# Optimization experiments

Hardware: AMD Instinct MI355X
Metric: run time of the kernel (lower is better)

The kernel has to match this reference:

```python
import jax, jax.numpy as jnp
import numpy as np

CODEBOOK_SIZE = 1024
CODEBOOK_DIM = 64
COMMITMENT_WEIGHT = 0.25
DECAY = 0.99
EPS = 1e-5


def setup_inputs() -> dict:
    key = jax.random.key(0)
    k1, k2, k3 = jax.random.split(key, 3)
    B, D, T = 32, CODEBOOK_DIM, 4096
    z = jax.random.normal(k1, (B, D, T), dtype=jnp.float32)
    embedding = jax.random.normal(k2, (CODEBOOK_SIZE, CODEBOOK_DIM), dtype=jnp.float32)
    cluster_size = jnp.zeros((CODEBOOK_SIZE,), dtype=jnp.float32)
    embed_avg = jax.random.normal(k3, (CODEBOOK_SIZE, CODEBOOK_DIM), dtype=jnp.float32)
    return {"z": z, "embedding": embedding, "cluster_size": cluster_size, "embed_avg": embed_avg}


def reference(z, embedding, cluster_size, embed_avg):
    # z: [B, D, T]; embedding/embed_avg: [K, D]; cluster_size: [K]
    B, D, T = z.shape
    K = embedding.shape[0]
    z_flat = jnp.transpose(z, (0, 2, 1)).reshape(-1, D)  # [N, D], N = B*T

    # squared-euclidean distances via expansion (matches torch cdist expansion)
    dist = (
        jnp.sum(z_flat * z_flat, axis=1, keepdims=True)
        + jnp.sum(embedding * embedding, axis=1)
        - 2.0 * (z_flat @ embedding.T)
    )  # [N, K]
    indices = jnp.argmin(dist, axis=1)  # [N] int

    # EMA updates (training path). one_hot.sum(0) -> segment count; one_hot.T @ z_flat -> segment sum
    counts = jax.ops.segment_sum(jnp.ones(z_flat.shape[0], dtype=z_flat.dtype), indices, num_segments=K)
    new_cluster_size = cluster_size * DECAY + (1.0 - DECAY) * counts
    embed_sum = jax.ops.segment_sum(z_flat, indices, num_segments=K)  # [K, D]
    new_embed_avg = embed_avg * DECAY + (1.0 - DECAY) * embed_sum
    n = jnp.sum(new_cluster_size)
    smoothed = (new_cluster_size + EPS) / (n + K * EPS) * n  # Laplace smoothing
    new_embedding = new_embed_avg / smoothed[:, None]  # [K, D]

    # quantize with the *updated* codebook (as in the torch in-place update)
    z_q_flat = new_embedding[indices]  # [N, D] gather
    loss = COMMITMENT_WEIGHT * jnp.mean((z_flat - jax.lax.stop_gradient(z_q_flat)) ** 2)
    # straight-through estimator
    z_q_flat = z_flat + jax.lax.stop_gradient(z_q_flat - z_flat)
    z_q = jnp.transpose(z_q_flat.reshape(B, T, D), (0, 2, 1))  # [B, D, T]
    return z_q, loss, indices.reshape(B, T)
```

## Files before the change

kernel.cpp:

```cpp
#include <hip/hip_runtime.h>

#define N_PTS 131072
#define TD 4096
#define DD 64
#define KK 1024
#define MARGIN_TH 2e-3f

typedef short bf16x8 __attribute__((ext_vector_type(8)));
typedef float f32x4  __attribute__((ext_vector_type(4)));

__device__ inline unsigned short f2bf(float f) {
    unsigned u = __float_as_uint(f);
    unsigned r = u + 0x7FFFu + ((u >> 16) & 1u);
    return (unsigned short)(r >> 16);
}
__device__ inline float bf2f(unsigned short h) {
    return __uint_as_float(((unsigned)h) << 16);
}

__global__ __launch_bounds__(256) void vq_prep(const float* __restrict__ z,
                                               unsigned short* __restrict__ zh,
                                               unsigned short* __restrict__ zl)
{
    __shared__ float tile[64][65];
    const int tid = threadIdx.x;
    const int b = blockIdx.x >> 6;
    const int t0 = (blockIdx.x & 63) * 64;

    const int d = tid >> 2, tq = tid & 3;
#pragma unroll
    for (int it = 0; it < 4; ++it) {
        const int tt = tq * 16 + it * 4;
        const float4 v = *(const float4*)(z + ((size_t)b * DD + d) * TD + t0 + tt);
        tile[d][tt] = v.x; tile[d][tt + 1] = v.y; tile[d][tt + 2] = v.z; tile[d][tt + 3] = v.w;
    }
    __syncthreads();

    const int p = tid >> 2, dg = tid & 3;
    bf16x8 h0, h1, l0, l1;
#pragma unroll
    for (int j = 0; j < 8; ++j) {
        const float v0 = -tile[dg * 16 + j][p];
        const unsigned short a = f2bf(v0);
        h0[j] = (short)a; l0[j] = (short)f2bf(v0 - bf2f(a));
        const float v1 = -tile[dg * 16 + 8 + j][p];
        const unsigned short c = f2bf(v1);
        h1[j] = (short)c; l1[j] = (short)f2bf(v1 - bf2f(c));
    }
    const size_t o = ((size_t)(b * TD + t0 + p)) * DD + dg * 16;
    *(bf16x8*)(zh + o) = h0;
    *(bf16x8*)(zh + o + 8) = h1;
    *(bf16x8*)(zl + o) = l0;
    *(bf16x8*)(zl + o + 8) = l1;
}

__global__ __launch_bounds__(256) void vq_eprep(const float* __restrict__ emb,
                                                unsigned short* __restrict__ efh,
                                                unsigned short* __restrict__ efl,
                                                float* __restrict__ halfnorm)
{
    const int k = blockIdx.x * 256 + threadIdx.x;
    if (k >= KK) return;
    const int t = k >> 4, col = k & 15;
    const float* e = emb + (size_t)k * DD;
    double s = 0.0;
#pragma unroll
    for (int d = 0; d < DD; ++d) {
        const float v = e[d];
        const double dv = (double)v;
        s = fma(dv, dv, s);
        const unsigned short h = f2bf(v);
        const int q = d >> 3, j = d & 7;
        const size_t pos = (size_t)t * 1024 + (q >> 2) * 512 + ((q & 3) * 16 + col) * 8 + j;
        efh[pos] = h;
        efl[pos] = f2bf(v - bf2f(h));
    }
    halfnorm[k] = (float)(0.5 * s);
}

__global__ __launch_bounds__(256, 6) void vq_screen_mfma(
    const unsigned short* __restrict__ zh, const unsigned short* __restrict__ zl,
    const unsigned short* __restrict__ efh, const unsigned short* __restrict__ efl,
    const float* __restrict__ hn,
    int* __restrict__ idx_ws, float* __restrict__ ind_out,
    int* __restrict__ nflag, int* __restrict__ flags)
{
    __shared__ __align__(16) unsigned short tiles[2][2048];

    const int tid  = threadIdx.x;
    const int lane = tid & 63;
    const int wv   = tid >> 6;
    const int quad = lane >> 4;
    const int col  = lane & 15;
    const int loff = lane * 8;
    const int pbase = blockIdx.x * 64 + wv * 16;

    const bf16x8* ph = (const bf16x8*)(zh + (size_t)(pbase + col) * DD + quad * 8);
    const bf16x8* pl = (const bf16x8*)(zl + (size_t)(pbase + col) * DD + quad * 8);
    const bf16x8 Ah0 = ph[0], Ah1 = ph[4];
    const bf16x8 Al0 = pl[0], Al1 = pl[4];

    const unsigned short* sg = (tid < 128) ? (efh + tid * 8) : (efl + (tid - 128) * 8);

    *(bf16x8*)(&tiles[0][tid * 8]) = *(const bf16x8*)(sg);
    float chn = hn[col];

    float best[4]  = {1e30f, 1e30f, 1e30f, 1e30f};
    float best2[4] = {1e30f, 1e30f, 1e30f, 1e30f};
    int   bidx[4]  = {0, 0, 0, 0};

    __syncthreads();

    for (int t = 0; t < KK / 16; ++t) {
        const int cur = t & 1;

        bf16x8 nr;
        float nhn = 0.f;
        if (t < 63) {
            nr = *(const bf16x8*)(sg + (size_t)(t + 1) * 1024);
            nhn = hn[(t + 1) * 16 + col];
        }

        const unsigned short* buf = &tiles[cur][0];
        const bf16x8 Bh0 = *(const bf16x8*)(buf + loff);
        const bf16x8 Bh1 = *(const bf16x8*)(buf + 512 + loff);
        const bf16x8 Bl0 = *(const bf16x8*)(buf + 1024 + loff);
        const bf16x8 Bl1 = *(const bf16x8*)(buf + 1536 + loff);

        if (t < 63) *(bf16x8*)(&tiles[cur ^ 1][tid * 8]) = nr;

        f32x4 p = {chn, chn, chn, chn};
        p = __builtin_amdgcn_mfma_f32_16x16x32_bf16(Ah0, Bh0, p, 0, 0, 0);
        p = __builtin_amdgcn_mfma_f32_16x16x32_bf16(Ah1, Bh1, p, 0, 0, 0);
        p = __builtin_amdgcn_mfma_f32_16x16x32_bf16(Al0, Bh0, p, 0, 0, 0);
        p = __builtin_amdgcn_mfma_f32_16x16x32_bf16(Al1, Bh1, p, 0, 0, 0);
        p = __builtin_amdgcn_mfma_f32_16x16x32_bf16(Ah0, Bl0, p, 0, 0, 0);
        p = __builtin_amdgcn_mfma_f32_16x16x32_bf16(Ah1, Bl1, p, 0, 0, 0);

        const int code = t * 16 + col;
#pragma unroll
        for (int r = 0; r < 4; ++r) {
            const float s = p[r];
            best2[r] = __builtin_amdgcn_fmed3f(best[r], best2[r], s);
            bidx[r] = (s < best[r]) ? code : bidx[r];
            best[r] = fminf(best[r], s);
        }

        __syncthreads();
        chn = nhn;
    }

#pragma unroll
    for (int off = 1; off < 16; off <<= 1) {
#pragma unroll
        for (int r = 0; r < 4; ++r) {
            const float ob  = __shfl_xor(best[r],  off, 64);
            const float ob2 = __shfl_xor(best2[r], off, 64);
            const int   oi  = __shfl_xor(bidx[r],  off, 64);
            const float nb2 = fminf(fminf(best2[r], ob2), fmaxf(best[r], ob));
            if (ob < best[r]) { best[r] = ob; bidx[r] = oi; }
            best2[r] = nb2;
        }
    }

    if (col == 0) {
#pragma unroll
        for (int r = 0; r < 4; ++r) {
            const int n0 = pbase + quad * 4 + r;
            idx_ws[n0] = bidx[r];
            ind_out[n0] = (float)bidx[r];
            if (best2[r] - best[r] < MARGIN_TH) {
                const int pos = atomicAdd(nflag, 1);
                flags[pos] = n0;
            }
        }
    }
}

__global__ __launch_bounds__(256) void vq_fallback(
    const float* __restrict__ z, const float* __restrict__ emb,
    int* __restrict__ idx_ws, float* __restrict__ ind_out,
    const int* __restrict__ nflag, const int* __restrict__ flags)
{
    __shared__ float zs[4][DD];
    const int total = *nflag;
    const int lane = threadIdx.x & 63;
    const int wid = threadIdx.x >> 6;
    const int gw = blockIdx.x * 4 + wid;

    for (int i = gw; i < total; i += gridDim.x * 4) {
        const int n = flags[i];
        const int b = n >> 12, t = n & 4095;
        zs[wid][lane] = z[((size_t)b * DD + lane) * TD + t];
        __builtin_amdgcn_s_waitcnt(0);
        double best = 1e300;
        int bi = KK;
        for (int kc = 0; kc < KK / 64; ++kc) {
            const int k = kc * 64 + lane;
            const float4* e = (const float4*)(emb + (size_t)k * DD);
            double dot = 0.0, nn = 0.0;
#pragma unroll
            for (int j = 0; j < 16; ++j) {
                float4 ev = e[j];
                double e0 = (double)ev.x, e1 = (double)ev.y, e2 = (double)ev.z, e3 = (double)ev.w;
                nn = fma(e0, e0, fma(e1, e1, fma(e2, e2, fma(e3, e3, nn))));
                dot = fma((double)zs[wid][4 * j + 0], e0,
                      fma((double)zs[wid][4 * j + 1], e1,
                      fma((double)zs[wid][4 * j + 2], e2,
                      fma((double)zs[wid][4 * j + 3], e3, dot))));
            }
            double s = 0.5 * nn - dot;
            if (s < best || (s == best && k < bi)) { best = s; bi = k; }
        }
        for (int off = 32; off > 0; off >>= 1) {
            double os = __shfl_down(best, off, 64);
            int oi = __shfl_down(bi, off, 64);
            if (os < best || (os == best && oi < bi)) { best = os; bi = oi; }
        }
        if (lane == 0) { idx_ws[n] = bi; ind_out[n] = (float)bi; }
    }
}

__global__ __launch_bounds__(256) void vq_hist(const int* __restrict__ idx_ws, int* __restrict__ hist)
{
    __shared__ int h[KK];
    for (int i = threadIdx.x; i < KK; i += 256) h[i] = 0;
    __syncthreads();
    const int base = blockIdx.x * 2048;
#pragma unroll
    for (int j = 0; j < 8; ++j)
        atomicAdd(&h[idx_ws[base + j * 256 + threadIdx.x]], 1);
    __syncthreads();
    for (int i = threadIdx.x; i < KK; i += 256)
        if (h[i]) atomicAdd(&hist[i], h[i]);
}

__global__ __launch_bounds__(1024) void vq_prefix_smo(
    const int* __restrict__ hist, const float* __restrict__ cs,
    int* __restrict__ cursor, float* __restrict__ rsmo)
{
    __shared__ int tmp[KK];
    __shared__ double dred[KK];
    const int k = threadIdx.x;
    const int c = hist[k];
    tmp[k] = c;
    const double ncs = 0.99 * (double)cs[k] + 0.01 * (double)c;
    dred[k] = ncs;
    __syncthreads();
    for (int off = 1; off < KK; off <<= 1) {
        int u = (k >= off) ? tmp[k - off] : 0;
        __syncthreads();
        tmp[k] += u;
        __syncthreads();
    }
    cursor[k] = tmp[k] - c;
    for (int s = 512; s > 0; s >>= 1) {
        if (k < s) dred[k] += dred[k + s];
        __syncthreads();
    }
    const double nsum = dred[0];
    const double smo = (ncs + 1e-5) / (nsum + (double)KK * 1e-5) * nsum;
    rsmo[k] = (float)(1.0 / smo);
}

__global__ __launch_bounds__(256) void vq_scatter(const int* __restrict__ idx_ws,
                                                  int* __restrict__ cursor, int* __restrict__ order)
{
    const int n = blockIdx.x * 256 + threadIdx.x;
    const int bi = idx_ws[n];
    const int pos = atomicAdd(&cursor[bi], 1);
    order[pos] = n;
}

__global__ __launch_bounds__(256) void vq_esum2(
    const unsigned short* __restrict__ zh, const unsigned short* __restrict__ zl,
    const int* __restrict__ idx_ws, const int* __restrict__ order,
    float* __restrict__ esum)
{
    const int tid = threadIdx.x;
    const int lane = tid & 63;
    const int w = tid >> 6;
    const int base = blockIdx.x * 256 + w * 64;

    const int pid_l = order[base + lane];
    const int code_l = idx_ws[pid_l];

    float v[64];
#pragma unroll
    for (int j = 0; j < 64; ++j) {
        const int pj = __shfl(pid_l, j, 64);
        const size_t o = (size_t)pj * DD + lane;
        v[j] = bf2f(zh[o]) + bf2f(zl[o]);
    }

    float racc = 0.f;
    int cur = __shfl(code_l, 0, 64);
#pragma unroll
    for (int j = 0; j < 64; ++j) {
        const int cj = __shfl(code_l, j, 64);
        if (cj != cur) {
            atomicAdd(&esum[(size_t)cur * DD + lane], -racc);
            racc = 0.f;
            cur = cj;
        }
        racc += v[j];
    }
    atomicAdd(&esum[(size_t)cur * DD + lane], -racc);
}

__global__ __launch_bounds__(256) void vq_newE(
    const float* __restrict__ avg, const float* __restrict__ esum,
    const float* __restrict__ rsmo, float* __restrict__ newE)
{
    const int j = blockIdx.x * 256 + threadIdx.x;
    newE[j] = (float)((0.99 * (double)avg[j] + 0.01 * (double)esum[j]) * (double)rsmo[j >> 6]);
}

__global__ __launch_bounds__(256) void vq_gather_loss(
    const float* __restrict__ z, const float* __restrict__ newE,
    const int* __restrict__ idx_ws, float* __restrict__ zq_out,
    double* __restrict__ loss_acc, int* __restrict__ done_cnt,
    float* __restrict__ loss_out)
{
    const int tid = threadIdx.x;
    const int n = blockIdx.x * 256 + tid;
    const int b = n >> 12;
    const int t = n & 4095;
    const float* zb = z + ((size_t)b * DD) * TD + t;
    float* ob = zq_out + ((size_t)b * DD) * TD + t;
    const int bi = idx_ws[n];
    const float* e = newE + (size_t)bi * DD;
    double acc = 0.0;
#pragma unroll
    for (int d = 0; d < DD; ++d) {
        float q = e[d];
        float zv = zb[(size_t)d * TD];
        ob[(size_t)d * TD] = q;
        float df = zv - q;
        acc = fma((double)df, (double)df, acc);
    }
    for (int off = 32; off > 0; off >>= 1) acc += __shfl_down(acc, off, 64);
    __shared__ double wsum[4];
    const int wid = tid >> 6, lane = tid & 63;
    if (lane == 0) wsum[wid] = acc;
    __syncthreads();
    if (tid == 0) {
        atomicAdd(loss_acc, wsum[0] + wsum[1] + wsum[2] + wsum[3]);
        __threadfence();
        const int prev = atomicAdd(done_cnt, 1);
        if (prev == gridDim.x - 1) {
            __threadfence();
            *loss_out = (float)(0.25 * (*loss_acc) / (double)(N_PTS * DD));
        }
    }
}

extern "C" void kernel_launch(void* const* d_in, const int* in_sizes, int n_in,
                              void* d_out, int out_size, void* d_ws, size_t ws_size,
                              hipStream_t stream) {
    const float* z    = (const float*)d_in[0];
    const float* emb  = (const float*)d_in[1];
    const float* cs   = (const float*)d_in[2];
    const float* avg  = (const float*)d_in[3];

    float* out      = (float*)d_out;
    float* zq_out   = out;
    float* loss_out = out + 8388608;
    float* ind_out  = out + 8388609;

    unsigned short* zh = (unsigned short*)d_out;
    unsigned short* zl = (unsigned short*)((char*)d_out + 16777216);

    char* ws = (char*)d_ws;
    int*            idx_ws   = (int*)ws;
    float*          newE     = (float*)(ws + 524288);
    float*          esum     = (float*)(ws + 786432);
    int*            hist     = (int*)(ws + 1048576);
    int*            nflag    = (int*)(ws + 1052672);
    int*            done_cnt = (int*)(ws + 1052676);
    double*         loss_acc = (double*)(ws + 1052680);
    float*          halfnorm = (float*)(ws + 1052688);
    int*            cursor   = (int*)(ws + 1056784);
    int*            flags    = (int*)(ws + 1060880);
    int*            order    = (int*)(ws + 1585168);
    unsigned short* efh      = (unsigned short*)(ws + 2109456);
    unsigned short* efl      = (unsigned short*)(ws + 2240528);
    float*          rsmo     = (float*)(ws + 2371600);

    hipMemsetAsync(ws + 786432, 0, 266256, stream);

    vq_prep<<<2048, 256, 0, stream>>>(z, zh, zl);
    vq_eprep<<<4, 256, 0, stream>>>(emb, efh, efl, halfnorm);
    vq_screen_mfma<<<N_PTS / 64, 256, 0, stream>>>(zh, zl, efh, efl, halfnorm,
                                                   idx_ws, ind_out, nflag, flags);
    vq_fallback<<<128, 256, 0, stream>>>(z, emb, idx_ws, ind_out, nflag, flags);
    vq_hist<<<64, 256, 0, stream>>>(idx_ws, hist);
    vq_prefix_smo<<<1, 1024, 0, stream>>>(hist, cs, cursor, rsmo);
    vq_scatter<<<N_PTS / 256, 256, 0, stream>>>(idx_ws, cursor, order);
    vq_esum2<<<N_PTS / 256, 256, 0, stream>>>(zh, zl, idx_ws, order, esum);
    vq_newE<<<256, 256, 0, stream>>>(avg, esum, rsmo, newE);
    vq_gather_loss<<<N_PTS / 256, 256, 0, stream>>>(z, newE, idx_ws, zq_out,
                                                    loss_acc, done_cnt, loss_out);
}
```

Baseline: 294.4 us.

## Use direct global-to-LDS loads with 4-deep staging and fuse codebook prep

The screening kernel now streams codebook tiles straight into LDS with global_load_lds across a 4-buffer ring. It keeps two tiles in flight and synchronises with vmcnt waits plus a single barrier per step, instead of a register round-trip and a trailing syncthreads. The half-norms are preloaded into shared memory once per block, and the codebook prep kernel is folded into vq_prep as extra blocks to save a launch. The cost is more LDS per block, which may limit occupancy, and the hand-written waitcnt ordering has to be correct.

```diff
diff --git a/kernel.cpp b/kernel.cpp
--- a/kernel.cpp
+++ b/kernel.cpp
@@ -18,12 +18,43 @@
     return __uint_as_float(((unsigned)h) << 16);
 }
 
+__device__ inline void gload_lds16(const unsigned short* g, unsigned short* l) {
+    __builtin_amdgcn_global_load_lds(
+        (const __attribute__((address_space(1))) unsigned int*)g,
+        (__attribute__((address_space(3))) unsigned int*)l, 16, 0, 0);
+}
+
 __global__ __launch_bounds__(256) void vq_prep(const float* __restrict__ z,
                                                unsigned short* __restrict__ zh,
-                                               unsigned short* __restrict__ zl)
+                                               unsigned short* __restrict__ zl,
+                                               const float* __restrict__ emb,
+                                               unsigned short* __restrict__ efh,
+                                               unsigned short* __restrict__ efl,
+                                               float* __restrict__ halfnorm)
 {
     __shared__ float tile[64][65];
     const int tid = threadIdx.x;
+
+    if (blockIdx.x >= 2048) {
+        const int k = (blockIdx.x - 2048) * 256 + tid;
+        const int t = k >> 4, col = k & 15;
+        const float* e = emb + (size_t)k * DD;
+        double s = 0.0;
+#pragma unroll
+        for (int d = 0; d < DD; ++d) {
+            const float v = e[d];
+            const double dv = (double)v;
+            s = fma(dv, dv, s);
+            const unsigned short h = f2bf(v);
+            const int q = d >> 3, j = d & 7;
+            const size_t pos = (size_t)t * 1024 + (q >> 2) * 512 + ((q & 3) * 16 + col) * 8 + j;
+            efh[pos] = h;
+            efl[pos] = f2bf(v - bf2f(h));
+        }
+        halfnorm[k] = (float)(0.5 * s);
+        return;
+    }
+
     const int b = blockIdx.x >> 6;
     const int t0 = (blockIdx.x & 63) * 64;
 
@@ -54,30 +85,6 @@
     *(bf16x8*)(zl + o + 8) = l1;
 }
 
-__global__ __launch_bounds__(256) void vq_eprep(const float* __restrict__ emb,
-                                                unsigned short* __restrict__ efh,
-                                                unsigned short* __restrict__ efl,
-                                                float* __restrict__ halfnorm)
-{
-    const int k = blockIdx.x * 256 + threadIdx.x;
-    if (k >= KK) return;
-    const int t = k >> 4, col = k & 15;
-    const float* e = emb + (size_t)k * DD;
-    double s = 0.0;
-#pragma unroll
-    for (int d = 0; d < DD; ++d) {
-        const float v = e[d];
-        const double dv = (double)v;
-        s = fma(dv, dv, s);
-        const unsigned short h = f2bf(v);
-        const int q = d >> 3, j = d & 7;
-        const size_t pos = (size_t)t * 1024 + (q >> 2) * 512 + ((q & 3) * 16 + col) * 8 + j;
-        efh[pos] = h;
-        efl[pos] = f2bf(v - bf2f(h));
-    }
-    halfnorm[k] = (float)(0.5 * s);
-}
-
 __global__ __launch_bounds__(256, 6) void vq_screen_mfma(
     const unsigned short* __restrict__ zh, const unsigned short* __restrict__ zl,
     const unsigned short* __restrict__ efh, const unsigned short* __restrict__ efl,
@@ -85,7 +92,8 @@
     int* __restrict__ idx_ws, float* __restrict__ ind_out,
     int* __restrict__ nflag, int* __restrict__ flags)
 {
-    __shared__ __align__(16) unsigned short tiles[2][2048];
+    __shared__ __align__(16) unsigned short tiles[4][2048];
+    __shared__ float hns[KK];
 
     const int tid  = threadIdx.x;
     const int lane = tid & 63;
@@ -100,55 +108,69 @@
     const bf16x8 Ah0 = ph[0], Ah1 = ph[4];
     const bf16x8 Al0 = pl[0], Al1 = pl[4];
 
+    ((float4*)hns)[tid] = ((const float4*)hn)[tid];
+
     const unsigned short* sg = (tid < 128) ? (efh + tid * 8) : (efl + (tid - 128) * 8);
 
-    *(bf16x8*)(&tiles[0][tid * 8]) = *(const bf16x8*)(sg);
-    float chn = hn[col];
+    asm volatile("s_waitcnt vmcnt(0)" ::: "memory");
+    __builtin_amdgcn_sched_barrier(0);
+    __syncthreads();
+
+#define STAGE(T) gload_lds16(sg + (size_t)(T) * 1024, &tiles[(T) & 3][tid * 8])
+
+    STAGE(0);
+    STAGE(1);
 
     float best[4]  = {1e30f, 1e30f, 1e30f, 1e30f};
     float best2[4] = {1e30f, 1e30f, 1e30f, 1e30f};
     int   bidx[4]  = {0, 0, 0, 0};
 
-    __syncthreads();
-
-    for (int t = 0; t < KK / 16; ++t) {
-        const int cur = t & 1;
-
-        bf16x8 nr;
-        float nhn = 0.f;
-        if (t < 63) {
-            nr = *(const bf16x8*)(sg + (size_t)(t + 1) * 1024);
-            nhn = hn[(t + 1) * 16 + col];
-        }
-
-        const unsigned short* buf = &tiles[cur][0];
-        const bf16x8 Bh0 = *(const bf16x8*)(buf + loff);
-        const bf16x8 Bh1 = *(const bf16x8*)(buf + 512 + loff);
-        const bf16x8 Bl0 = *(const bf16x8*)(buf + 1024 + loff);
-        const bf16x8 Bl1 = *(const bf16x8*)(buf + 1536 + loff);
-
-        if (t < 63) *(bf16x8*)(&tiles[cur ^ 1][tid * 8]) = nr;
-
-        f32x4 p = {chn, chn, chn, chn};
-        p = __builtin_amdgcn_mfma_f32_16x16x32_bf16(Ah0, Bh0, p, 0, 0, 0);
-        p = __builtin_amdgcn_mfma_f32_16x16x32_bf16(Ah1, Bh1, p, 0, 0, 0);
-        p = __builtin_amdgcn_mfma_f32_16x16x32_bf16(Al0, Bh0, p, 0, 0, 0);
-        p = __builtin_amdgcn_mfma_f32_16x16x32_bf16(Al1, Bh1, p, 0, 0, 0);
-        p = __builtin_amdgcn_mfma_f32_16x16x32_bf16(Ah0, Bl0, p, 0, 0, 0);
-        p = __builtin_amdgcn_mfma_f32_16x16x32_bf16(Ah1, Bl1, p, 0, 0, 0);
-
-        const int code = t * 16 + col;
-#pragma unroll
-        for (int r = 0; r < 4; ++r) {
-            const float s = p[r];
-            best2[r] = __builtin_amdgcn_fmed3f(best[r], best2[r], s);
-            bidx[r] = (s < best[r]) ? code : bidx[r];
-            best[r] = fminf(best[r], s);
-        }
-
-        __syncthreads();
-        chn = nhn;
-    }
+#define BODY(T)                                                                     \
+    {                                                                               \
+        const unsigned short* buf = &tiles[(T) & 3][0];                             \
+        const bf16x8 Bh0 = *(const bf16x8*)(buf + loff);                            \
+        const bf16x8 Bh1 = *(const bf16x8*)(buf + 512 + loff);                      \
+        const bf16x8 Bl0 = *(const bf16x8*)(buf + 1024 + loff);                     \
+        const bf16x8 Bl1 = *(const bf16x8*)(buf + 1536 + loff);                     \
+        const float chn = hns[(T) * 16 + col];                                      \
+        f32x4 p = {chn, chn, chn, chn};                                             \
+        p = __builtin_amdgcn_mfma_f32_16x16x32_bf16(Ah0, Bh0, p, 0, 0, 0);          \
+        p = __builtin_amdgcn_mfma_f32_16x16x32_bf16(Ah1, Bh1, p, 0, 0, 0);          \
+        p = __builtin_amdgcn_mfma_f32_16x16x32_bf16(Al0, Bh0, p, 0, 0, 0);          \
+        p = __builtin_amdgcn_mfma_f32_16x16x32_bf16(Al1, Bh1, p, 0, 0, 0);          \
+        p = __builtin_amdgcn_mfma_f32_16x16x32_bf16(Ah0, Bl0, p, 0, 0, 0);          \
+        p = __builtin_amdgcn_mfma_f32_16x16x32_bf16(Ah1, Bl1, p, 0, 0, 0);          \
+        const int code = (T) * 16 + col;                                            \
+        _Pragma("unroll")                                                           \
+        for (int r = 0; r < 4; ++r) {                                               \
+            const float s = p[r];                                                   \
+            best2[r] = __builtin_amdgcn_fmed3f(best[r], best2[r], s);               \
+            bidx[r] = (s < best[r]) ? code : bidx[r];                               \
+            best[r] = fminf(best[r], s);                                            \
+        }                                                                           \
+    }
+
+    for (int t = 0; t < 62; ++t) {
+        STAGE(t + 2);
+        asm volatile("s_waitcnt vmcnt(2)" ::: "memory");
+        __builtin_amdgcn_sched_barrier(0);
+        __builtin_amdgcn_s_barrier();
+        __builtin_amdgcn_sched_barrier(0);
+        BODY(t);
+    }
+    asm volatile("s_waitcnt vmcnt(1)" ::: "memory");
+    __builtin_amdgcn_sched_barrier(0);
+    __builtin_amdgcn_s_barrier();
+    __builtin_amdgcn_sched_barrier(0);
+    BODY(62);
+    asm volatile("s_waitcnt vmcnt(0)" ::: "memory");
+    __builtin_amdgcn_sched_barrier(0);
+    __builtin_amdgcn_s_barrier();
+    __builtin_amdgcn_sched_barrier(0);
+    BODY(63);
+
+#undef STAGE
+#undef BODY
 
 #pragma unroll
     for (int off = 1; off < 16; off <<= 1) {
@@ -389,8 +411,7 @@
 
     hipMemsetAsync(ws + 786432, 0, 266256, stream);
 
-    vq_prep<<<2048, 256, 0, stream>>>(z, zh, zl);
-    vq_eprep<<<4, 256, 0, stream>>>(emb, efh, efl, halfnorm);
+    vq_prep<<<2052, 256, 0, stream>>>(z, zh, zl, emb, efh, efl, halfnorm);
     vq_screen_mfma<<<N_PTS / 64, 256, 0, stream>>>(zh, zl, efh, efl, halfnorm,
                                                    idx_ws, ind_out, nflag, flags);
     vq_fallback<<<128, 256, 0, stream>>>(z, emb, idx_ws, ind_out, nflag, flags);
```

Result: faster. 287.0 us (-2.5%).
